# Kernel tuning notes

Hardware: AMD Instinct MI355X
Metric: run time of the kernel (lower is better)

Reference implementation:

```python
import jax, jax.numpy as jnp
import numpy as np
from jax import lax

B, C, H, W = 4, 96, 256, 256
EPS = 1e-12  # torch F.normalize default eps


def setup_inputs() -> dict:
    key = jax.random.key(0)
    ks = jax.random.split(key, 7)
    s1 = 1.0 / np.sqrt(C).astype(np.float32)
    x = jax.random.normal(ks[0], (B, C, H, W), dtype=jnp.float32)
    qkv_w = jax.random.normal(ks[1], (3 * C, C), dtype=jnp.float32) * s1      # 1x1 conv as matmul
    qkv_b = jax.random.normal(ks[2], (3 * C,), dtype=jnp.float32) * 0.01
    dw_w = jax.random.normal(ks[3], (3 * C, 1, 3, 3), dtype=jnp.float32) / 3.0  # depthwise 3x3
    dw_b = jax.random.normal(ks[4], (3 * C,), dtype=jnp.float32) * 0.01
    temp = jnp.ones((C, 1, 1), dtype=jnp.float32)                             # nn.Parameter(ones(dim,1,1))
    proj_w = jax.random.normal(ks[5], (C, C), dtype=jnp.float32) * s1
    proj_b = jax.random.normal(ks[6], (C,), dtype=jnp.float32) * 0.01
    return {"x": x, "qkv_w": qkv_w, "qkv_b": qkv_b, "dw_w": dw_w,
            "dw_b": dw_b, "temp": temp, "proj_w": proj_w, "proj_b": proj_b}


def _l2norm_h(t):
    # torch F.normalize(t, dim=-2): L2 over the H axis, eps-clamped denominator
    n = jnp.sqrt(jnp.sum(t * t, axis=-2, keepdims=True))
    return t / jnp.maximum(n, EPS)


def reference(x, qkv_w, qkv_b, dw_w, dw_b, temp, proj_w, proj_b):
    # 1x1 conv QKV projection
    qkv = jnp.einsum('bchw,oc->bohw', x, qkv_w) + qkv_b[None, :, None, None]
    # depthwise 3x3 conv (groups = 3C), padding 1
    qkv = lax.conv_general_dilated(
        qkv, dw_w, window_strides=(1, 1), padding='SAME',
        feature_group_count=qkv.shape[1],
        dimension_numbers=('NCHW', 'OIHW', 'NCHW')) + dw_b[None, :, None, None]
    q, k, v = jnp.split(qkv, 3, axis=1)  # each [B,C,H,W]
    q1 = _l2norm_h(q)
    k1 = _l2norm_h(k)
    # attn1 = (q1^T @ k1) * temperature : [B,C,W,W], temp broadcasts over (W,W)
    attn = jnp.einsum('bchw,bchv->bcwv', q1, k1) * temp[None]
    attn = jax.nn.softmax(attn, axis=-2)
    # out = v @ attn : [B,C,H,W]
    out = jnp.einsum('bchw,bcwv->bchv', v, attn)
    # 1x1 output projection
    out = jnp.einsum('bchw,oc->bohw', out, proj_w) + proj_b[None, :, None, None]
    return out
```

## Files before the change

kernel.cpp:

```cpp
#include <hip/hip_runtime.h>

#define NC 96
#define NC3 288
#define NH 256
#define NW 256
#define NHW 65536

typedef unsigned short ushort_t;
typedef __attribute__((ext_vector_type(8))) short bf16x8;
typedef __attribute__((ext_vector_type(4))) float f32x4;

__device__ __forceinline__ ushort_t f2bf(float x) {
  unsigned u = __float_as_uint(x);
  u += 0x7fffu + ((u >> 16) & 1u);
  return (ushort_t)(u >> 16);
}
__device__ __forceinline__ float bf2f(ushort_t h) {
  return __uint_as_float((unsigned)h << 16);
}
__device__ __forceinline__ unsigned pack_split(float f) {
  unsigned u = __float_as_uint(f);
  unsigned ur = u + (0x7fffu + ((u >> 16) & 1u));
  const float rem = f - __uint_as_float(ur & 0xffff0000u);
  unsigned v = __float_as_uint(rem);
  v += 0x7fffu + ((v >> 16) & 1u);
  return (ur >> 16) | (v & 0xffff0000u);
}
__device__ __forceinline__ float upk(unsigned u) {
  return __uint_as_float(u << 16) + __uint_as_float(u & 0xffff0000u);
}

__global__ __launch_bounds__(256) void k_wprep(
    const float* __restrict__ qkv_w, const float* __restrict__ proj_w,
    ushort_t* __restrict__ wq_hi, ushort_t* __restrict__ wq_lo,
    ushort_t* __restrict__ wp_hi, ushort_t* __restrict__ wp_lo) {
  const int id = blockIdx.x * 256 + threadIdx.x;
  if (id < NC3 * NC) {
    const float v = qkv_w[id];
    const ushort_t h = f2bf(v);
    wq_hi[id] = h;
    wq_lo[id] = f2bf(v - bf2f(h));
  } else {
    const int j = id - NC3 * NC;
    const float v = proj_w[j];
    const ushort_t h = f2bf(v);
    wp_hi[j] = h;
    wp_lo[j] = f2bf(v - bf2f(h));
  }
}

template <int OUTC, bool TILED>
__global__ __launch_bounds__(256, 3) void k_conv(
    const float* __restrict__ in, const ushort_t* __restrict__ w_hi,
    const ushort_t* __restrict__ w_lo, const float* __restrict__ bias,
    float* __restrict__ out) {
  __shared__ float xt[96][66];
  __shared__ __align__(16) ushort_t xh[64][104];
  __shared__ __align__(16) ushort_t xl[64][104];
  const int t = threadIdx.x;
  const int bz = blockIdx.y;
  const int sblk = blockIdx.x;
  const int s0 = sblk * 64;
  const float* xb = in + (size_t)bz * NC * NHW + s0;
#pragma unroll
  for (int i = 0; i < 6; ++i) {
    const int idx = t + 256 * i;
    const int row = idx >> 4, c4 = (idx & 15) << 2;
    *(float4*)&xt[row][c4] = *(const float4*)&xb[(size_t)row * NHW + c4];
  }

  const int lane = t & 63, wave = t >> 6;
  const int ln15 = lane & 15;
  const int akof = (lane >> 4) * 8;

  bf16x8 wH[2][6], wL[2][6];
#pragma unroll
  for (int m = 0; m < 6; ++m) {
    const int wi = (m * 16 + ln15) * NC + akof;
    wH[0][m] = *(const bf16x8*)(w_hi + wi);
    wL[0][m] = *(const bf16x8*)(w_lo + wi);
  }
  __syncthreads();
  {
    const int s = t & 63, cg = t >> 6;
#pragma unroll
    for (int i = 0; i < 12; ++i) {
      const int c = cg * 24 + i * 2;
      const float f0 = xt[c][s], f1 = xt[c + 1][s];
      const ushort_t h0 = f2bf(f0), h1 = f2bf(f1);
      const ushort_t l0 = f2bf(f0 - bf2f(h0)), l1 = f2bf(f1 - bf2f(h1));
      *(unsigned*)&xh[s][c] = (unsigned)h0 | ((unsigned)h1 << 16);
      *(unsigned*)&xl[s][c] = (unsigned)l0 | ((unsigned)l1 << 16);
    }
  }
  __syncthreads();
  bf16x8 bH[3], bL[3];
  {
    const int srow = wave * 16 + ln15;
#pragma unroll
    for (int kk = 0; kk < 3; ++kk) {
      bH[kk] = *(const bf16x8*)&xh[srow][kk * 32 + akof];
      bL[kk] = *(const bf16x8*)&xl[srow][kk * 32 + akof];
    }
  }

  constexpr int S = 3 * (OUTC / 96);
  const int sl = wave * 16 + ln15;
  f32x4 acc[6];
#pragma unroll
  for (int step = 0; step < S; ++step) {
    const int ocg = step / 3, kk = step % 3;
    if (kk == 0) {
#pragma unroll
      for (int m = 0; m < 6; ++m) acc[m] = (f32x4){0.f, 0.f, 0.f, 0.f};
    }
    if (step + 1 < S) {
      const int nocg = (step + 1) / 3, nkk = (step + 1) % 3;
#pragma unroll
      for (int m = 0; m < 6; ++m) {
        const int wi = (nocg * 96 + m * 16 + ln15) * NC + nkk * 32 + akof;
        wH[(step + 1) & 1][m] = *(const bf16x8*)(w_hi + wi);
        wL[(step + 1) & 1][m] = *(const bf16x8*)(w_lo + wi);
      }
    }
#pragma unroll
    for (int m = 0; m < 6; ++m) {
      const bf16x8 aH = wH[step & 1][m];
      const bf16x8 aL = wL[step & 1][m];
      acc[m] = __builtin_amdgcn_mfma_f32_16x16x32_bf16(aH, bH[kk], acc[m], 0, 0, 0);
      acc[m] = __builtin_amdgcn_mfma_f32_16x16x32_bf16(aH, bL[kk], acc[m], 0, 0, 0);
      acc[m] = __builtin_amdgcn_mfma_f32_16x16x32_bf16(aL, bH[kk], acc[m], 0, 0, 0);
    }
    if (kk == 2) {
      __syncthreads();
#pragma unroll
      for (int m = 0; m < 6; ++m) {
        const int o2 = m * 16 + (lane >> 4) * 4;
#pragma unroll
        for (int r = 0; r < 4; ++r) xt[o2 + r][sl] = acc[m][r];
      }
      __syncthreads();
      if (TILED) {
        unsigned* ob = (unsigned*)out +
                       ((size_t)(bz * 1024 + sblk)) * OUTC * 64 +
                       (size_t)ocg * 96 * 64;
#pragma unroll
        for (int j = 0; j < 6; ++j) {
          const int idx = t + 256 * j;
          const int row = idx >> 4, c4 = (idx & 15) << 2;
          const float bs = bias[ocg * 96 + row];
          uint4 pkv;
          pkv.x = pack_split(xt[row][c4 + 0] + bs);
          pkv.y = pack_split(xt[row][c4 + 1] + bs);
          pkv.z = pack_split(xt[row][c4 + 2] + bs);
          pkv.w = pack_split(xt[row][c4 + 3] + bs);
          *(uint4*)(ob + (size_t)row * 64 + c4) = pkv;
        }
      } else {
        float* ob = out + (size_t)bz * OUTC * NHW + s0;
#pragma unroll
        for (int j = 0; j < 6; ++j) {
          const int idx = t + 256 * j;
          const int row = idx >> 4, c4 = (idx & 15) << 2;
          const float bs = bias[ocg * 96 + row];
          const float4 v =
              make_float4(xt[row][c4] + bs, xt[row][c4 + 1] + bs,
                          xt[row][c4 + 2] + bs, xt[row][c4 + 3] + bs);
          *(float4*)(ob + (size_t)(ocg * 96 + row) * NHW + c4) = v;
        }
      }
    }
  }
}

__global__ __launch_bounds__(256, 8) void k_dw3(
    const unsigned* __restrict__ qkvt, const float* __restrict__ w,
    const float* __restrict__ bias, ushort_t* __restrict__ qt_hi,
    ushort_t* __restrict__ qt_lo, ushort_t* __restrict__ kt_hi,
    ushort_t* __restrict__ kt_lo, unsigned* __restrict__ v_pk,
    float* __restrict__ nq_p, float* __restrict__ nk_p) {
  __shared__ float sd[18][264];
  const int t = threadIdx.x;
  const int hb = blockIdx.x;
  const int bcc = blockIdx.y;
  const int b = bcc / NC3, ch = bcc % NC3;
  const int h0 = hb * 16;
  const unsigned* src = qkvt + (size_t)b * 1024 * NC3 * 64 + (size_t)ch * 64;
#pragma unroll
  for (int i = 0; i < 5; ++i) {
    const int idx = t + 256 * i;
    if (idx < 18 * 64) {
      const int r = idx >> 6, j = idx & 63;
      const int gh = h0 + r - 1;
      float4 v = make_float4(0.f, 0.f, 0.f, 0.f);
      if (gh >= 0 && gh < 256) {
        const int gw = 4 * j;
        const uint4 pv = *(const uint4*)&src[(size_t)(gh * 4 + (gw >> 6)) *
                                                 (NC3 * 64) +
                                             (gw & 63)];
        v = make_float4(upk(pv.x), upk(pv.y), upk(pv.z), upk(pv.w));
      }
      *(float4*)&sd[r][4 + 4 * j] = v;
    }
  }
  if (t < 36) {
    const int r = t >> 1;
    sd[r][(t & 1) ? 260 : 3] = 0.f;
  }
  __syncthreads();
  float wr[9];
#pragma unroll
  for (int k = 0; k < 9; ++k) wr[k] = w[ch * 9 + k];
  const float bs = bias[ch];
  const int wl = t;
  float res[16];
  float r0a = sd[0][wl + 3], r0b = sd[0][wl + 4], r0c = sd[0][wl + 5];
  float r1a = sd[1][wl + 3], r1b = sd[1][wl + 4], r1c = sd[1][wl + 5];
#pragma unroll
  for (int r = 0; r < 16; ++r) {
    const float r2a = sd[r + 2][wl + 3], r2b = sd[r + 2][wl + 4],
                r2c = sd[r + 2][wl + 5];
    float a = bs;
    a = fmaf(r0a, wr[0], a);
    a = fmaf(r0b, wr[1], a);
    a = fmaf(r0c, wr[2], a);
    a = fmaf(r1a, wr[3], a);
    a = fmaf(r1b, wr[4], a);
    a = fmaf(r1c, wr[5], a);
    a = fmaf(r2a, wr[6], a);
    a = fmaf(r2b, wr[7], a);
    a = fmaf(r2c, wr[8], a);
    res[r] = a;
    r0a = r1a; r0b = r1b; r0c = r1c;
    r1a = r2a; r1b = r2b; r1c = r2c;
  }
  if (ch < 192) {
    const int qk = ch / 96, c = ch - qk * 96;
    const int bc = b * 96 + c;
    float ss = 0.f;
#pragma unroll
    for (int r = 0; r < 16; ++r) ss = fmaf(res[r], res[r], ss);
    (qk ? nk_p : nq_p)[(size_t)bc * 4096 + hb * 256 + wl] = ss;
    const size_t tb = (size_t)bc * NHW + (hb >> 1) * 8192 + (size_t)wl * 32 +
                      (hb & 1) * 16;
    ushort_t* dh = (qk ? kt_hi : qt_hi) + tb;
    ushort_t* dl = (qk ? kt_lo : qt_lo) + tb;
#pragma unroll
    for (int j4 = 0; j4 < 2; ++j4) {
      uint4 H, L;
      unsigned* ph = (unsigned*)&H;
      unsigned* pl = (unsigned*)&L;
#pragma unroll
      for (int e = 0; e < 4; ++e) {
        const float f0 = res[j4 * 8 + 2 * e], f1 = res[j4 * 8 + 2 * e + 1];
        const ushort_t hh0 = f2bf(f0), hh1 = f2bf(f1);
        ph[e] = (unsigned)hh0 | ((unsigned)hh1 << 16);
        pl[e] = (unsigned)f2bf(f0 - bf2f(hh0)) |
                ((unsigned)f2bf(f1 - bf2f(hh1)) << 16);
      }
      *(uint4*)(dh + j4 * 8) = H;
      *(uint4*)(dl + j4 * 8) = L;
    }
  } else {
    const int bc = b * 96 + (ch - 192);
    const int wb = wl >> 5, wsub = wl & 31;
    unsigned* dp = v_pk + (size_t)bc * NHW + wb * 8192 + wsub;
#pragma unroll
    for (int r = 0; r < 16; ++r) {
      const float f = res[r];
      const ushort_t hh = f2bf(f);
      dp[(h0 + r) * 32] = (unsigned)hh | ((unsigned)f2bf(f - bf2f(hh)) << 16);
    }
  }
}

__global__ __launch_bounds__(256, 3) void k_attn_mfma(
    const ushort_t* __restrict__ qt_hi, const ushort_t* __restrict__ qt_lo,
    const ushort_t* __restrict__ kt_hi, const ushort_t* __restrict__ kt_lo,
    const float* __restrict__ nq_p, const float* __restrict__ nk_p,
    const float* __restrict__ temp, ushort_t* __restrict__ pt_hi,
    ushort_t* __restrict__ pt_lo) {
  __shared__ __align__(16) char smem[52480];
  ushort_t* qh = (ushort_t*)smem;
  ushort_t* ql = (ushort_t*)(smem + 20480);
  ushort_t* kh = (ushort_t*)(smem + 40960);
  ushort_t* kl = (ushort_t*)(smem + 46080);
  float* red = (float*)(smem + 51200);
  float* iqs = red;
  float* iks = (float*)(smem + 52224);
  ushort_t* pts = (ushort_t*)smem;

  const int t = threadIdx.x;
  const int lane = t & 63;
  const int wid = t >> 6;
  const int bid = blockIdx.x;
  const int pxb = gridDim.x >> 5;
  const int bc = (bid & 7) * pxb + (bid >> 5);
  const int v0 = ((bid >> 3) & 3) * 64;
  const size_t base_q = (size_t)bc * NHW;
  const size_t base_k = (size_t)bc * NHW + (size_t)v0 * 32;

  f32x4 acc[4][4];
#pragma unroll
  for (int mt = 0; mt < 4; ++mt)
#pragma unroll
    for (int nt = 0; nt < 4; ++nt) acc[mt][nt] = (f32x4){0.f, 0.f, 0.f, 0.f};

  for (int hb = 0; hb < 8; ++hb) {
    {
      const ushort_t* gq = qt_hi + base_q + hb * 8192 + t * 32;
      const ushort_t* gl = qt_lo + base_q + hb * 8192 + t * 32;
      uint4* dh = (uint4*)(qh + t * 40);
      uint4* dl = (uint4*)(ql + t * 40);
#pragma unroll
      for (int j = 0; j < 4; ++j) {
        dh[j] = *(const uint4*)(gq + j * 8);
        dl[j] = *(const uint4*)(gl + j * 8);
      }
      if (t < 64) {
        const ushort_t* gk = kt_hi + base_k + hb * 8192 + t * 32;
        uint4* dk = (uint4*)(kh + t * 40);
#pragma unroll
        for (int j = 0; j < 4; ++j) dk[j] = *(const uint4*)(gk + j * 8);
      } else if (t < 128) {
        const int r = t - 64;
        const ushort_t* gk = kt_lo + base_k + hb * 8192 + r * 32;
        uint4* dk = (uint4*)(kl + r * 40);
#pragma unroll
        for (int j = 0; j < 4; ++j) dk[j] = *(const uint4*)(gk + j * 8);
      }
    }
    __syncthreads();
    bf16x8 aH[4], aL[4];
#pragma unroll
    for (int mt = 0; mt < 4; ++mt) {
      const int off = (wid * 64 + mt * 16 + (lane & 15)) * 40 + (lane >> 4) * 8;
      aH[mt] = *(const bf16x8*)(qh + off);
      aL[mt] = *(const bf16x8*)(ql + off);
    }
#pragma unroll
    for (int nt = 0; nt < 4; ++nt) {
      const int off = (nt * 16 + (lane & 15)) * 40 + (lane >> 4) * 8;
      const bf16x8 bH = *(const bf16x8*)(kh + off);
      const bf16x8 bL = *(const bf16x8*)(kl + off);
#pragma unroll
      for (int mt = 0; mt < 4; ++mt) {
        acc[mt][nt] = __builtin_amdgcn_mfma_f32_16x16x32_bf16(aH[mt], bH, acc[mt][nt], 0, 0, 0);
        acc[mt][nt] = __builtin_amdgcn_mfma_f32_16x16x32_bf16(aH[mt], bL, acc[mt][nt], 0, 0, 0);
        acc[mt][nt] = __builtin_amdgcn_mfma_f32_16x16x32_bf16(aL[mt], bH, acc[mt][nt], 0, 0, 0);
      }
    }
    __syncthreads();
  }

  {
    float s8 = 0.f;
    const float* np = nq_p + (size_t)bc * 4096 + t;
#pragma unroll
    for (int hb = 0; hb < 16; ++hb) s8 += np[hb * 256];
    iqs[t] = 1.f / fmaxf(sqrtf(s8), 1e-12f);
    if (t < 64) {
      float sk8 = 0.f;
      const float* nk = nk_p + (size_t)bc * 4096 + v0 + t;
#pragma unroll
      for (int hb = 0; hb < 16; ++hb) sk8 += nk[hb * 256];
      iks[t] = temp[bc % NC] / fmaxf(sqrtf(sk8), 1e-12f);
    }
  }
  __syncthreads();
#pragma unroll
  for (int mt = 0; mt < 4; ++mt) {
    float iq4[4];
#pragma unroll
    for (int r = 0; r < 4; ++r)
      iq4[r] = iqs[wid * 64 + mt * 16 + (lane >> 4) * 4 + r];
#pragma unroll
    for (int nt = 0; nt < 4; ++nt) {
      const float ikv = iks[nt * 16 + (lane & 15)];
#pragma unroll
      for (int r = 0; r < 4; ++r) acc[mt][nt][r] *= iq4[r] * ikv;
    }
  }
  __syncthreads();

  float Mv[4], Sv[4];
#pragma unroll
  for (int nt = 0; nt < 4; ++nt) {
    float m = -3.4e38f;
#pragma unroll
    for (int mt = 0; mt < 4; ++mt)
#pragma unroll
      for (int r = 0; r < 4; ++r) m = fmaxf(m, acc[mt][nt][r]);
    m = fmaxf(m, __shfl_xor(m, 16));
    m = fmaxf(m, __shfl_xor(m, 32));
    if (lane < 16) red[wid * 64 + nt * 16 + lane] = m;
  }
  __syncthreads();
#pragma unroll
  for (int nt = 0; nt < 4; ++nt) {
    const int vl = nt * 16 + (lane & 15);
    Mv[nt] = fmaxf(fmaxf(red[vl], red[64 + vl]),
                   fmaxf(red[128 + vl], red[192 + vl]));
  }
  __syncthreads();
#pragma unroll
  for (int nt = 0; nt < 4; ++nt) {
    float s = 0.f;
#pragma unroll
    for (int mt = 0; mt < 4; ++mt)
#pragma unroll
      for (int r = 0; r < 4; ++r) {
        const float p = __expf(acc[mt][nt][r] - Mv[nt]);
        acc[mt][nt][r] = p;
        s += p;
      }
    s += __shfl_xor(s, 16);
    s += __shfl_xor(s, 32);
    if (lane < 16) red[wid * 64 + nt * 16 + lane] = s;
  }
  __syncthreads();
#pragma unroll
  for (int nt = 0; nt < 4; ++nt) {
    const int vl = nt * 16 + (lane & 15);
    Sv[nt] = 1.f / (red[vl] + red[64 + vl] + red[128 + vl] + red[192 + vl]);
  }
#pragma unroll
  for (int nt = 0; nt < 4; ++nt)
#pragma unroll
    for (int mt = 0; mt < 4; ++mt)
#pragma unroll
      for (int r = 0; r < 4; ++r) acc[mt][nt][r] *= Sv[nt];
  __syncthreads();

  for (int pass = 0; pass < 2; ++pass) {
#pragma unroll
    for (int nt = 0; nt < 4; ++nt)
#pragma unroll
      for (int mt = 0; mt < 4; ++mt) {
        ushort_t pk[4];
#pragma unroll
        for (int r = 0; r < 4; ++r) {
          const float p = acc[mt][nt][r];
          const ushort_t hi = f2bf(p);
          pk[r] = pass == 0 ? hi : f2bf(p - bf2f(hi));
        }
        const int v = nt * 16 + (lane & 15);
        const int wb2 = wid * 64 + mt * 16 + ((lane >> 4) << 2);
        *(ushort4*)(pts + v * 264 + wb2) =
            make_ushort4(pk[0], pk[1], pk[2], pk[3]);
      }
    __syncthreads();
    ushort_t* dst = pass == 0 ? pt_hi : pt_lo;
#pragma unroll
    for (int i = 0; i < 2; ++i) {
      const int cid = t + (i << 8);
      const int wb = cid >> 6, v = cid & 63;
      const ushort_t* sp = pts + v * 264 + wb * 32;
      ushort_t* d = dst + (size_t)bc * NHW + (size_t)wb * 8192 +
                    (size_t)(v0 + v) * 32;
#pragma unroll
      for (int j = 0; j < 4; ++j)
        *(uint4*)(d + j * 8) = *(const uint4*)(sp + j * 8);
    }
    __syncthreads();
  }
}

__global__ __launch_bounds__(256, 3) void k_av_mfma(
    const unsigned* __restrict__ v_pk, const ushort_t* __restrict__ pt_hi,
    const ushort_t* __restrict__ pt_lo, float* __restrict__ aout) {
  __shared__ __align__(16) ushort_t vh[128 * 40];
  __shared__ __align__(16) ushort_t vl[128 * 40];
  __shared__ __align__(16) ushort_t ph[128 * 40];
  __shared__ __align__(16) ushort_t pl[128 * 40];
  const int t = threadIdx.x;
  const int lane = t & 63;
  const int wid = t >> 6;
  const int bid = blockIdx.x;
  const int pxb = gridDim.x >> 5;
  const int bc = (bid & 7) * pxb + (bid >> 5);
  const int tile = (bid >> 3) & 3;
  const int h0 = (tile >> 1) * 128, v0 = (tile & 1) * 128;
  const int wh = wid >> 1, wv = wid & 1;

  f32x4 acc[4][4];
#pragma unroll
  for (int mt = 0; mt < 4; ++mt)
#pragma unroll
    for (int nt = 0; nt < 4; ++nt) acc[mt][nt] = (f32x4){0.f, 0.f, 0.f, 0.f};

  for (int wb = 0; wb < 8; ++wb) {
#pragma unroll
    for (int i = 0; i < 4; ++i) {
      const int id = t + (i << 8);
      const int row = id >> 3, q = id & 7;
      const uint4 pk = *(const uint4*)(v_pk + (size_t)bc * NHW + wb * 8192 +
                                       (size_t)(h0 + row) * 32 + q * 4);
      const ushort4 hi4 =
          make_ushort4((ushort_t)(pk.x & 0xffff), (ushort_t)(pk.y & 0xffff),
                       (ushort_t)(pk.z & 0xffff), (ushort_t)(pk.w & 0xffff));
      const ushort4 lo4 =
          make_ushort4((ushort_t)(pk.x >> 16), (ushort_t)(pk.y >> 16),
                       (ushort_t)(pk.z >> 16), (ushort_t)(pk.w >> 16));
      *(ushort4*)(vh + row * 40 + q * 4) = hi4;
      *(ushort4*)(vl + row * 40 + q * 4) = lo4;
    }
#pragma unroll
    for (int i = 0; i < 4; ++i) {
      const int id = t + (i << 8);
      const int arr = id >> 9, rem = id & 511;
      const int row = rem >> 2, q = rem & 3;
      const ushort_t* g = (arr ? pt_lo : pt_hi) + (size_t)bc * NHW +
                          wb * 8192 + (size_t)(v0 + row) * 32 + q * 8;
      ushort_t* d = (arr ? pl : ph) + row * 40 + q * 8;
      *(uint4*)d = *(const uint4*)g;
    }
    __syncthreads();
    bf16x8 aH[4], aL[4];
#pragma unroll
    for (int mt = 0; mt < 4; ++mt) {
      const int off = (wh * 64 + mt * 16 + (lane & 15)) * 40 + (lane >> 4) * 8;
      aH[mt] = *(const bf16x8*)(vh + off);
      aL[mt] = *(const bf16x8*)(vl + off);
    }
#pragma unroll
    for (int nt = 0; nt < 4; ++nt) {
      const int off = (wv * 64 + nt * 16 + (lane & 15)) * 40 + (lane >> 4) * 8;
      const bf16x8 bH = *(const bf16x8*)(ph + off);
      const bf16x8 bL = *(const bf16x8*)(pl + off);
#pragma unroll
      for (int mt = 0; mt < 4; ++mt) {
        acc[mt][nt] = __builtin_amdgcn_mfma_f32_16x16x32_bf16(aH[mt], bH, acc[mt][nt], 0, 0, 0);
        acc[mt][nt] = __builtin_amdgcn_mfma_f32_16x16x32_bf16(aH[mt], bL, acc[mt][nt], 0, 0, 0);
        acc[mt][nt] = __builtin_amdgcn_mfma_f32_16x16x32_bf16(aL[mt], bH, acc[mt][nt], 0, 0, 0);
      }
    }
    __syncthreads();
  }

#pragma unroll
  for (int mt = 0; mt < 4; ++mt) {
    const int hbase = h0 + wh * 64 + mt * 16 + ((lane >> 4) << 2);
#pragma unroll
    for (int nt = 0; nt < 4; ++nt) {
      const int vv = v0 + wv * 64 + nt * 16 + (lane & 15);
      float* o = aout + (size_t)bc * NHW + (size_t)hbase * NW + vv;
#pragma unroll
      for (int r = 0; r < 4; ++r) o[(size_t)r * NW] = acc[mt][nt][r];
    }
  }
}

extern "C" void kernel_launch(void* const* d_in, const int* in_sizes, int n_in,
                              void* d_out, int out_size, void* d_ws,
                              size_t ws_size, hipStream_t stream) {
  const float* x = (const float*)d_in[0];
  const float* qkv_w = (const float*)d_in[1];
  const float* qkv_b = (const float*)d_in[2];
  const float* dw_w = (const float*)d_in[3];
  const float* dw_b = (const float*)d_in[4];
  const float* temp = (const float*)d_in[5];
  const float* proj_w = (const float*)d_in[6];
  const float* proj_b = (const float*)d_in[7];
  float* out = (float*)d_out;

  auto need = [](int nb) -> size_t {
    return (size_t)nb * 154140672ull + 147456ull;
  };
  int nb = 1;
  if (need(4) <= ws_size) nb = 4;
  else if (need(2) <= ws_size) nb = 2;

  char* base = (char*)d_ws;
  const size_t QKV_T = (size_t)nb * 75497472ull;
  const size_t HALF = (size_t)nb * 12582912ull;
  const size_t NQB = (size_t)nb * 1572864ull;
  unsigned* qkv_tiled = (unsigned*)base;
  ushort_t* pt_hi = (ushort_t*)base;
  ushort_t* pt_lo = (ushort_t*)(base + HALF);
  float* aout = (float*)(base + 2 * HALF);
  char* p = base + QKV_T;
  ushort_t* qt_hi = (ushort_t*)p; p += HALF;
  ushort_t* qt_lo = (ushort_t*)p; p += HALF;
  ushort_t* kt_hi = (ushort_t*)p; p += HALF;
  ushort_t* kt_lo = (ushort_t*)p; p += HALF;
  unsigned* v_pk = (unsigned*)p; p += 2 * HALF;
  float* nq_p = (float*)p; p += NQB;
  float* nk_p = (float*)p; p += NQB;
  ushort_t* wq_hi = (ushort_t*)p; p += 55296;
  ushort_t* wq_lo = (ushort_t*)p; p += 55296;
  ushort_t* wp_hi = (ushort_t*)p; p += 18432;
  ushort_t* wp_lo = (ushort_t*)p;

  k_wprep<<<dim3(144), 256, 0, stream>>>(qkv_w, proj_w, wq_hi, wq_lo, wp_hi, wp_lo);

  const int BC = nb * NC;
  for (int b0 = 0; b0 < 4; b0 += nb) {
    const float* xb = x + (size_t)b0 * NC * NHW;
    float* outb = out + (size_t)b0 * NC * NHW;
    k_conv<NC3, true><<<dim3(1024, nb), 256, 0, stream>>>(
        xb, wq_hi, wq_lo, qkv_b, (float*)qkv_tiled);
    k_dw3<<<dim3(16, nb * NC3), 256, 0, stream>>>(
        qkv_tiled, dw_w, dw_b, qt_hi, qt_lo, kt_hi, kt_lo, v_pk, nq_p, nk_p);
    k_attn_mfma<<<dim3(BC * 4), 256, 0, stream>>>(
        qt_hi, qt_lo, kt_hi, kt_lo, nq_p, nk_p, temp, pt_hi, pt_lo);
    k_av_mfma<<<dim3(BC * 4), 256, 0, stream>>>(v_pk, pt_hi, pt_lo, aout);
    k_conv<NC, false><<<dim3(1024, nb), 256, 0, stream>>>(
        aout, wp_hi, wp_lo, proj_b, outb);
  }
}
```

Before: 569.6 us.

## Shrink conv LDS and registers for higher occupancy; change q/k tile layout

The 1x1 conv kernel now stages the input in two 48-channel halves through a smaller shared buffer that is aliased with the epilogue scratch. It drops the double-buffered weight registers and loads weights directly before each MFMA, and raises launch bounds from 3 to 4 blocks per CU. Separately, the depthwise kernel now writes q/k tiles in 16-row blocks instead of 32-row blocks, and the attention kernel gathers two such blocks per step. The aim is more resident waves to hide memory latency, at the cost of an extra barrier and less weight prefetching.

```diff
diff --git a/kernel.cpp b/kernel.cpp
--- a/kernel.cpp
+++ b/kernel.cpp
@@ -50,47 +50,48 @@
 }
 
 template <int OUTC, bool TILED>
-__global__ __launch_bounds__(256, 3) void k_conv(
+__global__ __launch_bounds__(256, 4) void k_conv(
     const float* __restrict__ in, const ushort_t* __restrict__ w_hi,
     const ushort_t* __restrict__ w_lo, const float* __restrict__ bias,
     float* __restrict__ out) {
-  __shared__ float xt[96][66];
-  __shared__ __align__(16) ushort_t xh[64][104];
-  __shared__ __align__(16) ushort_t xl[64][104];
+  __shared__ __align__(16) char smem[39936];
+  ushort_t* xh = (ushort_t*)smem;
+  ushort_t* xl = (ushort_t*)(smem + 13312);
+  float* xt48 = (float*)(smem + 26624);
+  float* est = (float*)smem;
   const int t = threadIdx.x;
   const int bz = blockIdx.y;
   const int sblk = blockIdx.x;
   const int s0 = sblk * 64;
   const float* xb = in + (size_t)bz * NC * NHW + s0;
-#pragma unroll
-  for (int i = 0; i < 6; ++i) {
-    const int idx = t + 256 * i;
-    const int row = idx >> 4, c4 = (idx & 15) << 2;
-    *(float4*)&xt[row][c4] = *(const float4*)&xb[(size_t)row * NHW + c4];
-  }
 
   const int lane = t & 63, wave = t >> 6;
   const int ln15 = lane & 15;
   const int akof = (lane >> 4) * 8;
 
-  bf16x8 wH[2][6], wL[2][6];
-#pragma unroll
-  for (int m = 0; m < 6; ++m) {
-    const int wi = (m * 16 + ln15) * NC + akof;
-    wH[0][m] = *(const bf16x8*)(w_hi + wi);
-    wL[0][m] = *(const bf16x8*)(w_lo + wi);
-  }
-  __syncthreads();
-  {
-    const int s = t & 63, cg = t >> 6;
-#pragma unroll
-    for (int i = 0; i < 12; ++i) {
-      const int c = cg * 24 + i * 2;
-      const float f0 = xt[c][s], f1 = xt[c + 1][s];
-      const ushort_t h0 = f2bf(f0), h1 = f2bf(f1);
-      const ushort_t l0 = f2bf(f0 - bf2f(h0)), l1 = f2bf(f1 - bf2f(h1));
-      *(unsigned*)&xh[s][c] = (unsigned)h0 | ((unsigned)h1 << 16);
-      *(unsigned*)&xl[s][c] = (unsigned)l0 | ((unsigned)l1 << 16);
+#pragma unroll 1
+  for (int half = 0; half < 2; ++half) {
+    if (half) __syncthreads();
+#pragma unroll
+    for (int i = 0; i < 3; ++i) {
+      const int idx = t + 256 * i;
+      const int row = idx >> 4, c4 = (idx & 15) << 2;
+      *(float4*)&xt48[row * 68 + c4] =
+          *(const float4*)&xb[(size_t)(half * 48 + row) * NHW + c4];
+    }
+    __syncthreads();
+    {
+      const int s = t & 63, cg = t >> 6;
+#pragma unroll
+      for (int i = 0; i < 6; ++i) {
+        const int cl = cg * 12 + i * 2;
+        const float f0 = xt48[cl * 68 + s], f1 = xt48[(cl + 1) * 68 + s];
+        const ushort_t h0 = f2bf(f0), h1 = f2bf(f1);
+        const ushort_t l0 = f2bf(f0 - bf2f(h0)), l1 = f2bf(f1 - bf2f(h1));
+        const int c = half * 48 + cl;
+        *(unsigned*)&xh[s * 104 + c] = (unsigned)h0 | ((unsigned)h1 << 16);
+        *(unsigned*)&xl[s * 104 + c] = (unsigned)l0 | ((unsigned)l1 << 16);
+      }
     }
   }
   __syncthreads();
@@ -99,8 +100,8 @@
     const int srow = wave * 16 + ln15;
 #pragma unroll
     for (int kk = 0; kk < 3; ++kk) {
-      bH[kk] = *(const bf16x8*)&xh[srow][kk * 32 + akof];
-      bL[kk] = *(const bf16x8*)&xl[srow][kk * 32 + akof];
+      bH[kk] = *(const bf16x8*)&xh[srow * 104 + kk * 32 + akof];
+      bL[kk] = *(const bf16x8*)&xl[srow * 104 + kk * 32 + akof];
     }
   }
 
@@ -114,19 +115,11 @@
 #pragma unroll
       for (int m = 0; m < 6; ++m) acc[m] = (f32x4){0.f, 0.f, 0.f, 0.f};
     }
-    if (step + 1 < S) {
-      const int nocg = (step + 1) / 3, nkk = (step + 1) % 3;
-#pragma unroll
-      for (int m = 0; m < 6; ++m) {
-        const int wi = (nocg * 96 + m * 16 + ln15) * NC + nkk * 32 + akof;
-        wH[(step + 1) & 1][m] = *(const bf16x8*)(w_hi + wi);
-        wL[(step + 1) & 1][m] = *(const bf16x8*)(w_lo + wi);
-      }
-    }
 #pragma unroll
     for (int m = 0; m < 6; ++m) {
-      const bf16x8 aH = wH[step & 1][m];
-      const bf16x8 aL = wL[step & 1][m];
+      const int wi = (ocg * 96 + m * 16 + ln15) * NC + kk * 32 + akof;
+      const bf16x8 aH = *(const bf16x8*)(w_hi + wi);
+      const bf16x8 aL = *(const bf16x8*)(w_lo + wi);
       acc[m] = __builtin_amdgcn_mfma_f32_16x16x32_bf16(aH, bH[kk], acc[m], 0, 0, 0);
       acc[m] = __builtin_amdgcn_mfma_f32_16x16x32_bf16(aH, bL[kk], acc[m], 0, 0, 0);
       acc[m] = __builtin_amdgcn_mfma_f32_16x16x32_bf16(aL, bH[kk], acc[m], 0, 0, 0);
@@ -137,7 +130,7 @@
       for (int m = 0; m < 6; ++m) {
         const int o2 = m * 16 + (lane >> 4) * 4;
 #pragma unroll
-        for (int r = 0; r < 4; ++r) xt[o2 + r][sl] = acc[m][r];
+        for (int r = 0; r < 4; ++r) est[(o2 + r) * 66 + sl] = acc[m][r];
       }
       __syncthreads();
       if (TILED) {
@@ -150,10 +143,10 @@
           const int row = idx >> 4, c4 = (idx & 15) << 2;
           const float bs = bias[ocg * 96 + row];
           uint4 pkv;
-          pkv.x = pack_split(xt[row][c4 + 0] + bs);
-          pkv.y = pack_split(xt[row][c4 + 1] + bs);
-          pkv.z = pack_split(xt[row][c4 + 2] + bs);
-          pkv.w = pack_split(xt[row][c4 + 3] + bs);
+          pkv.x = pack_split(est[row * 66 + c4 + 0] + bs);
+          pkv.y = pack_split(est[row * 66 + c4 + 1] + bs);
+          pkv.z = pack_split(est[row * 66 + c4 + 2] + bs);
+          pkv.w = pack_split(est[row * 66 + c4 + 3] + bs);
           *(uint4*)(ob + (size_t)row * 64 + c4) = pkv;
         }
       } else {
@@ -163,9 +156,9 @@
           const int idx = t + 256 * j;
           const int row = idx >> 4, c4 = (idx & 15) << 2;
           const float bs = bias[ocg * 96 + row];
-          const float4 v =
-              make_float4(xt[row][c4] + bs, xt[row][c4 + 1] + bs,
-                          xt[row][c4 + 2] + bs, xt[row][c4 + 3] + bs);
+          const float4 v = make_float4(
+              est[row * 66 + c4] + bs, est[row * 66 + c4 + 1] + bs,
+              est[row * 66 + c4 + 2] + bs, est[row * 66 + c4 + 3] + bs);
           *(float4*)(ob + (size_t)(ocg * 96 + row) * NHW + c4) = v;
         }
       }
@@ -241,8 +234,7 @@
 #pragma unroll
     for (int r = 0; r < 16; ++r) ss = fmaf(res[r], res[r], ss);
     (qk ? nk_p : nq_p)[(size_t)bc * 4096 + hb * 256 + wl] = ss;
-    const size_t tb = (size_t)bc * NHW + (hb >> 1) * 8192 + (size_t)wl * 32 +
-                      (hb & 1) * 16;
+    const size_t tb = (size_t)bc * NHW + (size_t)hb * 4096 + (size_t)wl * 16;
     ushort_t* dh = (qk ? kt_hi : qt_hi) + tb;
     ushort_t* dl = (qk ? kt_lo : qt_lo) + tb;
 #pragma unroll
@@ -298,7 +290,7 @@
   const int bc = (bid & 7) * pxb + (bid >> 5);
   const int v0 = ((bid >> 3) & 3) * 64;
   const size_t base_q = (size_t)bc * NHW;
-  const size_t base_k = (size_t)bc * NHW + (size_t)v0 * 32;
+  const size_t base_k = (size_t)bc * NHW;
 
   f32x4 acc[4][4];
 #pragma unroll
@@ -308,26 +300,39 @@
 
   for (int hb = 0; hb < 8; ++hb) {
     {
-      const ushort_t* gq = qt_hi + base_q + hb * 8192 + t * 32;
-      const ushort_t* gl = qt_lo + base_q + hb * 8192 + t * 32;
+      const ushort_t* g0 = qt_hi + base_q + (size_t)(2 * hb) * 4096 + t * 16;
+      const ushort_t* g1 = g0 + 4096;
+      const ushort_t* gl0 = qt_lo + base_q + (size_t)(2 * hb) * 4096 + t * 16;
+      const ushort_t* gl1 = gl0 + 4096;
       uint4* dh = (uint4*)(qh + t * 40);
       uint4* dl = (uint4*)(ql + t * 40);
-#pragma unroll
-      for (int j = 0; j < 4; ++j) {
-        dh[j] = *(const uint4*)(gq + j * 8);
-        dl[j] = *(const uint4*)(gl + j * 8);
-      }
+      dh[0] = *(const uint4*)(g0);
+      dh[1] = *(const uint4*)(g0 + 8);
+      dh[2] = *(const uint4*)(g1);
+      dh[3] = *(const uint4*)(g1 + 8);
+      dl[0] = *(const uint4*)(gl0);
+      dl[1] = *(const uint4*)(gl0 + 8);
+      dl[2] = *(const uint4*)(gl1);
+      dl[3] = *(const uint4*)(gl1 + 8);
       if (t < 64) {
-        const ushort_t* gk = kt_hi + base_k + hb * 8192 + t * 32;
+        const ushort_t* k0 =
+            kt_hi + base_k + (size_t)(2 * hb) * 4096 + (size_t)(v0 + t) * 16;
+        const ushort_t* k1 = k0 + 4096;
         uint4* dk = (uint4*)(kh + t * 40);
-#pragma unroll
-        for (int j = 0; j < 4; ++j) dk[j] = *(const uint4*)(gk + j * 8);
+        dk[0] = *(const uint4*)(k0);
+        dk[1] = *(const uint4*)(k0 + 8);
+        dk[2] = *(const uint4*)(k1);
+        dk[3] = *(const uint4*)(k1 + 8);
       } else if (t < 128) {
         const int r = t - 64;
-        const ushort_t* gk = kt_lo + base_k + hb * 8192 + r * 32;
+        const ushort_t* k0 =
+            kt_lo + base_k + (size_t)(2 * hb) * 4096 + (size_t)(v0 + r) * 16;
+        const ushort_t* k1 = k0 + 4096;
         uint4* dk = (uint4*)(kl + r * 40);
-#pragma unroll
-        for (int j = 0; j < 4; ++j) dk[j] = *(const uint4*)(gk + j * 8);
+        dk[0] = *(const uint4*)(k0);
+        dk[1] = *(const uint4*)(k0 + 8);
+        dk[2] = *(const uint4*)(k1);
+        dk[3] = *(const uint4*)(k1 + 8);
       }
     }
     __syncthreads();
```

Measured after the change: 519.7 us. 8.8% less time.
